# Kernel tuning notes

Measured on AMD Instinct MI355X. Metric: run time of the kernel, lower is better.

## Reference

```python
import jax, jax.numpy as jnp
import numpy as np

# irreps structure: in = 32x0e + 16x1o, hidden = 64x0e + 32x1o, out = 32x0e + 16x1o
N = 50000
S_IN, V_IN = 32, 16
S_H, V_H = 64, 32
S_OUT, V_OUT = 32, 16
INV_SQRT3 = float(1.0 / np.sqrt(3.0))  # wigner-3j for (0,1,1)/(1,0,1)/(1,1,0)
# e3nn path weights: sqrt(ir_out.dim / sum_over_paths_to_same_output(fan_in)), fan_in = mul1*mul2
PW1_S = float((1.0 / (S_IN * S_IN + V_IN * V_IN)) ** 0.5)        # sqrt(1/1280)
PW1_V = float((3.0 / (S_IN * V_IN + V_IN * S_IN)) ** 0.5)        # sqrt(3/1024)
PW2_S = float((1.0 / (S_H * S_H + V_H * V_H)) ** 0.5)            # sqrt(1/5120)
PW2_V = float((3.0 / (S_H * V_H + V_H * S_H)) ** 0.5)            # sqrt(3/4096)


def norm_act(xs, xv, bias=None, normalize=False):
    # e3nn.nn.NormActivation with sigmoid: per-irrep-channel norm, gate by sigmoid(norm [+ bias])
    ns = jnp.abs(xs)                                 # [N, S] scalar channel norms
    nv = jnp.sqrt(jnp.sum(xv * xv, axis=-1))         # [N, V] vector channel norms
    norms = jnp.concatenate([ns, nv], axis=1)        # [N, S+V]
    a = norms if bias is None else norms + bias
    f = jax.nn.sigmoid(a)
    mult = f / norms if normalize else f
    s = xs.shape[1]
    return xs * mult[:, :s], xv * mult[:, s:, None]


def fctp(xs, xv, Wsss, Wvvs, Wsvv, Wvsv, pw_s, pw_v):
    # FullyConnectedTensorProduct(x, x) restricted to 0e/1o irreps (all surviving CG paths)
    zs = pw_s * (jnp.einsum('nu,nv,uvw->nw', xs, xs, Wsss)
                 + INV_SQRT3 * jnp.einsum('nui,nvi,uvw->nw', xv, xv, Wvvs))
    zv = (pw_v * INV_SQRT3) * (jnp.einsum('nu,nvk,uvw->nwk', xs, xv, Wsvv)
                               + jnp.einsum('nuk,nv,uvw->nwk', xv, xs, Wvsv))
    return zs, zv


def setup_inputs() -> dict:
    key = jax.random.key(0)
    ks = jax.random.split(key, 11)
    return {
        'x': jax.random.normal(ks[0], (N, S_IN + 3 * V_IN), dtype=jnp.float32),
        'Wsss1': jax.random.normal(ks[1], (S_IN, S_IN, S_H), dtype=jnp.float32),
        'Wvvs1': jax.random.normal(ks[2], (V_IN, V_IN, S_H), dtype=jnp.float32),
        'Wsvv1': jax.random.normal(ks[3], (S_IN, V_IN, V_H), dtype=jnp.float32),
        'Wvsv1': jax.random.normal(ks[4], (V_IN, S_IN, V_H), dtype=jnp.float32),
        'Wsss2': jax.random.normal(ks[5], (S_H, S_H, S_OUT), dtype=jnp.float32),
        'Wvvs2': jax.random.normal(ks[6], (V_H, V_H, S_OUT), dtype=jnp.float32),
        'Wsvv2': jax.random.normal(ks[7], (S_H, V_H, V_OUT), dtype=jnp.float32),
        'Wvsv2': jax.random.normal(ks[8], (V_H, S_H, V_OUT), dtype=jnp.float32),
        'b1': 0.1 * jax.random.normal(ks[9], (S_IN + V_IN,), dtype=jnp.float32),
        'b3': 0.1 * jax.random.normal(ks[10], (S_OUT + V_OUT,), dtype=jnp.float32),
    }


def reference(x, Wsss1, Wvvs1, Wsvv1, Wvsv1, Wsss2, Wvvs2, Wsvv2, Wvsv2, b1, b3):
    xs = x[:, :S_IN]
    xv = x[:, S_IN:].reshape(-1, V_IN, 3)
    xs, xv = norm_act(xs, xv, bias=b1, normalize=False)            # non_linear_act1
    hs, hv = fctp(xs, xv, Wsss1, Wvvs1, Wsvv1, Wvsv1, PW1_S, PW1_V)  # si1
    hs, hv = norm_act(hs, hv, bias=None, normalize=True)           # normalize_and_non_linear_act2
    os_, ov = fctp(hs, hv, Wsss2, Wvvs2, Wsvv2, Wvsv2, PW2_S, PW2_V)  # si2
    os_, ov = norm_act(os_, ov, bias=b3, normalize=False)          # non_linear_act3
    return jnp.concatenate([os_, ov.reshape(-1, V_OUT * 3)], axis=1)
```

## Files before the change

kernel.cpp:

```cpp
#include <hip/hip_runtime.h>

#define NROWS 50000

typedef float f32x4 __attribute__((ext_vector_type(4)));
typedef float f32x16 __attribute__((ext_vector_type(16)));
typedef short s16x8 __attribute__((ext_vector_type(8)));
typedef _Float16 f16x8 __attribute__((ext_vector_type(8)));

#define MFMA16B(a,b,c) __builtin_amdgcn_mfma_f32_16x16x32_bf16(a, b, c, 0, 0, 0)
#define MFMA32B(a,b,c) __builtin_amdgcn_mfma_f32_32x32x16_bf16(a, b, c, 0, 0, 0)
#define MFMA32H(a,b,c) __builtin_amdgcn_mfma_f32_32x32x16_f16(a, b, c, 0, 0, 0)

#define Q1ABH 0
#define Q1ABL 81920
#define Q1CH  163840
#define Q1CL  212992
#define P2A   262144
#define P2C   425984
#define PREPN 393216


#define LO_SCALE   2048.0f
#define LO_UNSCALE 4.8828125e-4f

__device__ __forceinline__ float sigm(float a){ return 1.0f/(1.0f+__expf(-a)); }
__device__ __forceinline__ short bfb(float f){
  __bf16 b = (__bf16)f;
  return *reinterpret_cast<short*>(&b);
}
__device__ __forceinline__ float b2f(short s){
  unsigned u = ((unsigned)(unsigned short)s) << 16;
  float f;
  __builtin_memcpy(&f, &u, 4);
  return f;
}
__device__ __forceinline__ f32x16 zero16(){
  f32x16 v;
  #pragma unroll
  for (int i = 0; i < 16; ++i) v[i] = 0.f;
  return v;
}

__global__ __launch_bounds__(256) void prep_weights(
    const float* __restrict__ Wsss1, const float* __restrict__ Wvvs1,
    const float* __restrict__ Wsvv1, const float* __restrict__ Wvsv1,
    const float* __restrict__ Wsss2, const float* __restrict__ Wvvs2,
    const float* __restrict__ Wsvv2, const float* __restrict__ Wvsv2,
    short* __restrict__ pb)
{
  const float PW1S = 0.027950849718747374f;
  const float PW2S = 0.013975424859373687f;
  const float IS3  = 0.57735026918962576f;
  int i = blockIdx.x * 256 + threadIdx.x;
  if (i >= PREPN) return;
  if (i < 131072) {
    float w;
    int hiOff, loOff;
    if (i < 81920) {
      int e = i; int j = e & 7, l = (e >> 3) & 63, st = e >> 9;
      int t = st & 1, s = st >> 1;
      int k = 16*s + 8*(l >> 5) + j, n = 32*t + (l & 31);
      if (k < 1024) { int u = k >> 5, v = k & 31; w = PW1S * Wsss1[(u*32 + v)*64 + n]; }
      else { int kk = k - 1024; int u = kk >> 4, v = kk & 15; w = PW1S * IS3 * Wvvs1[(u*16 + v)*64 + n]; }
      hiOff = Q1ABH + e; loOff = Q1ABL + e;
    } else {
      int e = i - 81920; int e2 = e & 16383;
      int j = e2 & 7, l = (e2 >> 3) & 63, s = e2 >> 9;
      int k = 16*s + 8*(l >> 5) + j, n = l & 31;
      int u = k >> 4, v = k & 15;
      w = 0.03125f * (Wsvv1[(u*16 + v)*32 + n] + Wvsv1[(v*32 + u)*32 + n]);
      hiOff = Q1CH + e; loOff = Q1CL + e;
    }
    _Float16 h = (_Float16)w;
    float r = w - (float)h;
    _Float16 lo = (_Float16)(r * LO_SCALE);
    pb[hiOff] = *reinterpret_cast<short*>(&h);
    pb[loOff] = *reinterpret_cast<short*>(&lo);
  } else {
    int e = i - 131072;
    float val; int off;
    if (e < 163840) {
      int j = e & 7, l = (e >> 3) & 63, s = e >> 9;
      int k = 16*s + 8*(l >> 5) + j, n = l & 31;
      if (k < 4096) { int u = k >> 6, v = k & 63; val = PW2S * Wsss2[(u*64 + v)*32 + n]; }
      else { int kk = k - 4096; int u = kk >> 5, v = kk & 31; val = PW2S * IS3 * Wvvs2[(u*32 + v)*32 + n]; }
      off = P2A + e;
    } else {
      int e3 = e - 163840; int e4 = e3 & 32767;
      int j = e4 & 7, l = (e4 >> 3) & 63, s = e4 >> 9;
      int k = 32*s + 8*(l >> 4) + j, n = l & 15;
      int u = k >> 5, v = k & 31;
      val = 0.015625f * (Wsvv2[(u*32 + v)*16 + n] + Wvsv2[(v*64 + u)*16 + n]);
      off = P2C + e3;
    }
    pb[off] = bfb(val);
  }
}

__global__ __launch_bounds__(128, 4) void double_layer(
    const float* __restrict__ x,
    const float* __restrict__ b1,
    const float* __restrict__ b3,
    const short* __restrict__ pb,
    float* __restrict__ out)
{
  __shared__ __align__(16) float smem[5120];
  char* S = (char*)smem;

  const int lane = threadIdx.x & 63;
  const int wid  = __builtin_amdgcn_readfirstlane(threadIdx.x >> 6);
  const int h    = lane >> 5;
  const int r31  = lane & 31;
  const int row  = r31;
  const int grow0 = blockIdx.x * 32;
  const int xb = row * 320;
  const int hb = 10240 + row * 320;
  const int sz = ((row >> 1) & 3) << 4;
  const bool valid = (grow0 + row) < NROWS;
  const float* xrow = x + (size_t)(grow0 + row) * 80;

  if (wid == 0) {
    #pragma unroll
    for (int i = 0; i < 4; ++i) {
      float4 qv = valid ? ((const float4*)xrow)[4*h + i] : float4{0.f,0.f,0.f,0.f};
      int c0 = 16*h + 4*i;
      f32x4 o;
      o[0] = qv.x * sigm(fabsf(qv.x) + b1[c0+0]);
      o[1] = qv.y * sigm(fabsf(qv.y) + b1[c0+1]);
      o[2] = qv.z * sigm(fabsf(qv.z) + b1[c0+2]);
      o[3] = qv.w * sigm(fabsf(qv.w) + b1[c0+3]);
      *(f32x4*)(S + xb + ((64*h + 16*i) ^ sz)) = o;
    }
  } else {
    float t[24];
    #pragma unroll
    for (int i = 0; i < 6; ++i) {
      float4 qv = valid ? ((const float4*)xrow)[8 + 6*h + i] : float4{0.f,0.f,0.f,0.f};
      t[4*i] = qv.x; t[4*i+1] = qv.y; t[4*i+2] = qv.z; t[4*i+3] = qv.w;
    }
    #pragma unroll
    for (int vv = 0; vv < 8; ++vv) {
      float a0 = t[3*vv], a1 = t[3*vv+1], a2 = t[3*vv+2];
      float f = sigm(sqrtf(a0*a0 + a1*a1 + a2*a2) + b1[32 + 8*h + vv]);
      t[3*vv] = a0*f; t[3*vv+1] = a1*f; t[3*vv+2] = a2*f;
    }
    #pragma unroll
    for (int i = 0; i < 6; ++i) {
      f32x4 o; o[0] = t[4*i]; o[1] = t[4*i+1]; o[2] = t[4*i+2]; o[3] = t[4*i+3];
      *(f32x4*)(S + xb + ((128 + 96*h + 16*i) ^ sz)) = o;
    }
  }
  __syncthreads();

  if (wid == 0) {
    f32x16 aH0 = zero16(), aM0 = zero16(), aH1 = zero16(), aM1 = zero16();
    const f16x8* BH = (const f16x8*)(pb + Q1ABH);
    const f16x8* BL = (const f16x8*)(pb + Q1ABL);
    float xsv[16];
    {
      #pragma unroll
      for (int si = 0; si < 2; ++si) {
        f32x4 p0 = *(const f32x4*)(S + xb + ((64*si + 32*h) ^ sz));
        f32x4 p1 = *(const f32x4*)(S + xb + ((64*si + 32*h + 16) ^ sz));
        #pragma unroll
        for (int j = 0; j < 4; ++j) { xsv[8*si+j] = p0[j]; xsv[8*si+4+j] = p1[j]; }
      }
    }
    #pragma unroll 2
    for (int so = 0; so < 32; ++so) {
      float xu = *(const float*)(S + xb + ((4*so) ^ sz));
      #pragma unroll
      for (int si = 0; si < 2; ++si) {
        int s = 2*so + si;
        f16x8 ah, al;
        #pragma unroll
        for (int j = 0; j < 8; ++j) {
          float f = xu * xsv[8*si + j];
          _Float16 hh = (_Float16)f;
          ah[j] = hh;
          al[j] = (_Float16)((f - (float)hh) * LO_SCALE);
        }
        const f16x8* Bh = BH + (2*s)*64 + lane;
        const f16x8* Bl = BL + (2*s)*64 + lane;
        f16x8 b0 = Bh[0], b1_ = Bh[64];
        aH0 = MFMA32H(ah, b0,  aH0); aM0 = MFMA32H(al, b0,  aM0); aM0 = MFMA32H(ah, Bl[0],  aM0);
        aH1 = MFMA32H(ah, b1_, aH1); aM1 = MFMA32H(al, b1_, aM1); aM1 = MFMA32H(ah, Bl[64], aM1);
      }
    }
    {
      float pv0[8], pv1[8], pv2[8];
      f32x4 P[6];
      #pragma unroll
      for (int i = 0; i < 6; ++i) P[i] = *(const f32x4*)(S + xb + ((128 + 96*h + 16*i) ^ sz));
      #pragma unroll
      for (int j = 0; j < 8; ++j) {
        pv0[j] = P[(3*j  )>>2][(3*j  )&3];
        pv1[j] = P[(3*j+1)>>2][(3*j+1)&3];
        pv2[j] = P[(3*j+2)>>2][(3*j+2)&3];
      }
      #pragma unroll 2
      for (int s2 = 0; s2 < 16; ++s2) {
        int s = 64 + s2;
        float u0 = *(const float*)(S + xb + ((4*(32 + 3*s2    )) ^ sz));
        float u1 = *(const float*)(S + xb + ((4*(32 + 3*s2 + 1)) ^ sz));
        float u2 = *(const float*)(S + xb + ((4*(32 + 3*s2 + 2)) ^ sz));
        f16x8 ah, al;
        #pragma unroll
        for (int j = 0; j < 8; ++j) {
          float f = u0*pv0[j] + u1*pv1[j] + u2*pv2[j];
          _Float16 hh = (_Float16)f;
          ah[j] = hh;
          al[j] = (_Float16)((f - (float)hh) * LO_SCALE);
        }
        const f16x8* Bh = BH + (2*s)*64 + lane;
        const f16x8* Bl = BL + (2*s)*64 + lane;
        f16x8 b0 = Bh[0], b1_ = Bh[64];
        aH0 = MFMA32H(ah, b0,  aH0); aM0 = MFMA32H(al, b0,  aM0); aM0 = MFMA32H(ah, Bl[0],  aM0);
        aH1 = MFMA32H(ah, b1_, aH1); aM1 = MFMA32H(al, b1_, aM1); aM1 = MFMA32H(ah, Bl[64], aM1);
      }
    }
    #pragma unroll
    for (int reg = 0; reg < 16; ++reg) {
      int rowD = (reg & 3) + 8*(reg >> 2) + 4*h;
      int hbD = 10240 + rowD*320;
      int szD = ((rowD >> 1) & 3) << 4;
      float z0 = aH0[reg] + LO_UNSCALE*aM0[reg];
      float z1 = aH1[reg] + LO_UNSCALE*aM1[reg];
      *(short*)(S + hbD + ((2*r31)        ^ szD)) = bfb(copysignf(sigm(fabsf(z0)), z0));
      *(short*)(S + hbD + ((2*(32 + r31)) ^ szD)) = bfb(copysignf(sigm(fabsf(z1)), z1));
    }
  } else {
    float pv0[8], pv1[8], pv2[8];
    {
      f32x4 P[6];
      #pragma unroll
      for (int i = 0; i < 6; ++i) P[i] = *(const f32x4*)(S + xb + ((128 + 96*h + 16*i) ^ sz));
      #pragma unroll
      for (int j = 0; j < 8; ++j) {
        pv0[j] = P[(3*j  )>>2][(3*j  )&3];
        pv1[j] = P[(3*j+1)>>2][(3*j+1)&3];
        pv2[j] = P[(3*j+2)>>2][(3*j+2)&3];
      }
    }
    const f16x8* CH = (const f16x8*)(pb + Q1CH);
    const f16x8* CL = (const f16x8*)(pb + Q1CL);
    f32x16 z0v, z1v, z2v;
    {
      f32x16 cH0 = zero16(), cM0 = zero16(), cH1 = zero16(), cM1 = zero16();
      #pragma unroll 2
      for (int s = 0; s < 32; ++s) {
        float xu = *(const float*)(S + xb + ((4*s) ^ sz));
        f16x8 a0h, a0l, a1h, a1l;
        #pragma unroll
        for (int j = 0; j < 8; ++j) {
          float f0 = xu*pv0[j]; _Float16 h0 = (_Float16)f0; a0h[j] = h0; a0l[j] = (_Float16)((f0 - (float)h0)*LO_SCALE);
          float f1 = xu*pv1[j]; _Float16 h1 = (_Float16)f1; a1h[j] = h1; a1l[j] = (_Float16)((f1 - (float)h1)*LO_SCALE);
        }
        const f16x8* B0h = CH + s*64 + lane;
        const f16x8* B0l = CL + s*64 + lane;
        f16x8 t0 = B0h[0];
        cH0 = MFMA32H(a0h, t0, cH0); cM0 = MFMA32H(a0l, t0, cM0); cM0 = MFMA32H(a0h, B0l[0], cM0);
        f16x8 t1 = B0h[2048];
        cH1 = MFMA32H(a1h, t1, cH1); cM1 = MFMA32H(a1l, t1, cM1); cM1 = MFMA32H(a1h, B0l[2048], cM1);
      }
      #pragma unroll
      for (int i = 0; i < 16; ++i) { z0v[i] = cH0[i] + LO_UNSCALE*cM0[i]; z1v[i] = cH1[i] + LO_UNSCALE*cM1[i]; }
    }
    {
      f32x16 cH2 = zero16(), cM2 = zero16();
      #pragma unroll 2
      for (int s = 0; s < 32; ++s) {
        float xu = *(const float*)(S + xb + ((4*s) ^ sz));
        f16x8 a2h, a2l;
        #pragma unroll
        for (int j = 0; j < 8; ++j) {
          float f2 = xu*pv2[j]; _Float16 h2 = (_Float16)f2; a2h[j] = h2; a2l[j] = (_Float16)((f2 - (float)h2)*LO_SCALE);
        }
        const f16x8* B2h = CH + 4096 + s*64 + lane;
        const f16x8* B2l = CL + 4096 + s*64 + lane;
        f16x8 t2 = B2h[0];
        cH2 = MFMA32H(a2h, t2, cH2); cM2 = MFMA32H(a2l, t2, cM2); cM2 = MFMA32H(a2h, B2l[0], cM2);
      }
      #pragma unroll
      for (int i = 0; i < 16; ++i) z2v[i] = cH2[i] + LO_UNSCALE*cM2[i];
    }
    #pragma unroll
    for (int reg = 0; reg < 16; ++reg) {
      int rowD = (reg & 3) + 8*(reg >> 2) + 4*h;
      int hbD = 10240 + rowD*320;
      int szD = ((rowD >> 1) & 3) << 4;
      float a0 = z0v[reg], a1 = z1v[reg], a2 = z2v[reg];
      float n = sqrtf(a0*a0 + a1*a1 + a2*a2);
      float mm = sigm(n) / n;
      int ch = 64 + 3*r31;
      *(short*)(S + hbD + ((2*(ch    )) ^ szD)) = bfb(a0*mm);
      *(short*)(S + hbD + ((2*(ch + 1)) ^ szD)) = bfb(a1*mm);
      *(short*)(S + hbD + ((2*(ch + 2)) ^ szD)) = bfb(a2*mm);
    }
  }
  __syncthreads();

  if (wid == 0) {
    f32x16 acc = zero16();
    const s16x8* BA = (const s16x8*)(pb + P2A);
    {
      float hsv[32];
      #pragma unroll
      for (int p = 0; p < 4; ++p) {
        s16x8 w = *(const s16x8*)(S + hb + ((32*p + 16*h) ^ sz));
        #pragma unroll
        for (int j = 0; j < 8; ++j) hsv[8*p + j] = b2f(w[j]);
      }
      #pragma unroll 2
      for (int uu = 0; uu < 64; ++uu) {
        float hu = b2f(*(const short*)(S + hb + ((2*uu) ^ sz)));
        #pragma unroll
        for (int p = 0; p < 4; ++p) {
          s16x8 a;
          #pragma unroll
          for (int j = 0; j < 8; ++j) a[j] = bfb(hu * hsv[8*p + j]);
          acc = MFMA32B(a, BA[(4*uu + p)*64 + lane], acc);
        }
      }
    }
    {
      float hvv[48];
      #pragma unroll
      for (int p = 0; p < 2; ++p) {
        #pragma unroll
        for (int i = 0; i < 3; ++i) {
          s16x8 w = *(const s16x8*)(S + hb + ((128 + 96*p + 48*h + 16*i) ^ sz));
          #pragma unroll
          for (int j = 0; j < 8; ++j) hvv[24*p + 8*i + j] = b2f(w[j]);
        }
      }
      #pragma unroll 2
      for (int uu = 0; uu < 32; ++uu) {
        float u0 = b2f(*(const short*)(S + hb + ((2*(64 + 3*uu    )) ^ sz)));
        float u1 = b2f(*(const short*)(S + hb + ((2*(64 + 3*uu + 1)) ^ sz)));
        float u2 = b2f(*(const short*)(S + hb + ((2*(64 + 3*uu + 2)) ^ sz)));
        #pragma unroll
        for (int p = 0; p < 2; ++p) {
          s16x8 a;
          #pragma unroll
          for (int j = 0; j < 8; ++j) {
            float e0 = hvv[24*p + 3*j    ];
            float e1 = hvv[24*p + 3*j + 1];
            float e2 = hvv[24*p + 3*j + 2];
            a[j] = bfb(u0*e0 + u1*e1 + u2*e2);
          }
          acc = MFMA32B(a, BA[(256 + 2*uu + p)*64 + lane], acc);
        }
      }
    }
    float bs = b3[r31];
    #pragma unroll
    for (int reg = 0; reg < 16; ++reg) {
      int rowD = (reg & 3) + 8*(reg >> 2) + 4*h;
      int grow = grow0 + rowD;
      if (grow < NROWS) {
        float z = acc[reg];
        out[(size_t)grow*80 + r31] = z * sigm(fabsf(z) + bs);
      }
    }
  } else {
    const int q = lane >> 4, r15 = lane & 15;
    const int rA = r15, rB = 16 + r15;
    const int hbA = 10240 + rA*320, szA = ((rA >> 1) & 3) << 4;
    const int hbB = 10240 + rB*320, szB = ((rB >> 1) & 3) << 4;
    float vvA[24], vvB[24];
    #pragma unroll
    for (int i = 0; i < 3; ++i) {
      s16x8 wa = *(const s16x8*)(S + hbA + ((128 + 48*q + 16*i) ^ szA));
      s16x8 wb = *(const s16x8*)(S + hbB + ((128 + 48*q + 16*i) ^ szB));
      #pragma unroll
      for (int j = 0; j < 8; ++j) { vvA[8*i+j] = b2f(wa[j]); vvB[8*i+j] = b2f(wb[j]); }
    }
    f32x4 ac00 = {0.f,0.f,0.f,0.f}, ac01 = {0.f,0.f,0.f,0.f};
    f32x4 ac10 = {0.f,0.f,0.f,0.f}, ac11 = {0.f,0.f,0.f,0.f};
    f32x4 ac20 = {0.f,0.f,0.f,0.f}, ac21 = {0.f,0.f,0.f,0.f};
    const s16x8* BC = (const s16x8*)(pb + P2C);
    #pragma unroll 2
    for (int s = 0; s < 64; ++s) {
      float huA = b2f(*(const short*)(S + hbA + ((2*s) ^ szA)));
      float huB = b2f(*(const short*)(S + hbB + ((2*s) ^ szB)));
      s16x8 aA0, aA1, aA2, aB0, aB1, aB2;
      #pragma unroll
      for (int j = 0; j < 8; ++j) {
        aA0[j] = bfb(huA*vvA[3*j  ]); aA1[j] = bfb(huA*vvA[3*j+1]); aA2[j] = bfb(huA*vvA[3*j+2]);
        aB0[j] = bfb(huB*vvB[3*j  ]); aB1[j] = bfb(huB*vvB[3*j+1]); aB2[j] = bfb(huB*vvB[3*j+2]);
      }
      s16x8 B0 = BC[s*64 + lane];
      s16x8 B1 = BC[4096 + s*64 + lane];
      s16x8 B2 = BC[8192 + s*64 + lane];
      ac00 = MFMA16B(aA0, B0, ac00); ac01 = MFMA16B(aB0, B0, ac01);
      ac10 = MFMA16B(aA1, B1, ac10); ac11 = MFMA16B(aB1, B1, ac11);
      ac20 = MFMA16B(aA2, B2, ac20); ac21 = MFMA16B(aB2, B2, ac21);
    }
    float bv = b3[32 + r15];
    #pragma unroll
    for (int r = 0; r < 4; ++r) {
      int gA = grow0 + 4*q + r;
      if (gA < NROWS) {
        float z0 = ac00[r], z1 = ac10[r], z2 = ac20[r];
        float gg = sigm(sqrtf(z0*z0 + z1*z1 + z2*z2) + bv);
        out[(size_t)gA*80 + 32 + 3*r15    ] = z0*gg;
        out[(size_t)gA*80 + 32 + 3*r15 + 1] = z1*gg;
        out[(size_t)gA*80 + 32 + 3*r15 + 2] = z2*gg;
      }
      int gB = grow0 + 16 + 4*q + r;
      if (gB < NROWS) {
        float z0 = ac01[r], z1 = ac11[r], z2 = ac21[r];
        float gg = sigm(sqrtf(z0*z0 + z1*z1 + z2*z2) + bv);
        out[(size_t)gB*80 + 32 + 3*r15    ] = z0*gg;
        out[(size_t)gB*80 + 32 + 3*r15 + 1] = z1*gg;
        out[(size_t)gB*80 + 32 + 3*r15 + 2] = z2*gg;
      }
    }
  }
}

extern "C" void kernel_launch(void* const* d_in, const int* in_sizes, int n_in,
                              void* d_out, int out_size, void* d_ws, size_t ws_size,
                              hipStream_t stream) {
  const float* x     = (const float*)d_in[0];
  const float* Wsss1 = (const float*)d_in[1];
  const float* Wvvs1 = (const float*)d_in[2];
  const float* Wsvv1 = (const float*)d_in[3];
  const float* Wvsv1 = (const float*)d_in[4];
  const float* Wsss2 = (const float*)d_in[5];
  const float* Wvvs2 = (const float*)d_in[6];
  const float* Wsvv2 = (const float*)d_in[7];
  const float* Wvsv2 = (const float*)d_in[8];
  const float* b1    = (const float*)d_in[9];
  const float* b3    = (const float*)d_in[10];
  float* out = (float*)d_out;
  short* pb  = (short*)d_ws;

  hipLaunchKernelGGL(prep_weights, dim3((PREPN + 255)/256), dim3(256), 0, stream,
                     Wsss1, Wvvs1, Wsvv1, Wvsv1, Wsss2, Wvvs2, Wsvv2, Wvsv2, pb);
  hipLaunchKernelGGL(double_layer, dim3((NROWS + 31)/32), dim3(128), 0, stream,
                     x, b1, b3, pb, out);
}
```

Measured before the change: 122.1 us.

## Exploit symmetry of quadratic form in layer-2 scalar path to halve MFMAs

Because the scalar output of the second tensor product is a symmetric quadratic form in h (h_u h_v W_uvw), the prep kernel now folds W[u,v]+W[v,u] into upper-triangular 8x8 blocks. The wave-0 scalar path then iterates only over blocks with a<=b, for both the scalar-scalar and vector-vector parts. This roughly halves the MFMA count and the weight bytes loaded for that path. In exchange it adds a triangular block index decode in the prep kernel and a non-unrolled inner loop with a variable trip count in the main kernel.

```diff
diff --git a/kernel.cpp b/kernel.cpp
--- a/kernel.cpp
+++ b/kernel.cpp
@@ -16,8 +16,9 @@
 #define Q1CH  163840
 #define Q1CL  212992
 #define P2A   262144
+#define P2AV  (262144 + 73728)
 #define P2C   425984
-#define PREPN 393216
+#define PREPN 323584
 
 
 #define LO_SCALE   2048.0f
@@ -79,14 +80,31 @@
   } else {
     int e = i - 131072;
     float val; int off;
-    if (e < 163840) {
+    if (e < 73728) {
       int j = e & 7, l = (e >> 3) & 63, s = e >> 9;
       int k = 16*s + 8*(l >> 5) + j, n = l & 31;
-      if (k < 4096) { int u = k >> 6, v = k & 63; val = PW2S * Wsss2[(u*64 + v)*32 + n]; }
-      else { int kk = k - 4096; int u = kk >> 5, v = kk & 31; val = PW2S * IS3 * Wvvs2[(u*32 + v)*32 + n]; }
+      int B = k >> 6, kb = k & 63;
+      int bb = 0;
+      while ((bb + 1) * (bb + 2) / 2 <= B) ++bb;
+      int a = B - bb * (bb + 1) / 2;
+      int u = 8*a + (kb >> 3), v = 8*bb + (kb & 7);
+      float w1 = Wsss2[(u*64 + v)*32 + n];
+      val = PW2S * (a == bb ? w1 : w1 + Wsss2[(v*64 + u)*32 + n]);
       off = P2A + e;
+    } else if (e < 94208) {
+      int e2 = e - 73728;
+      int j = e2 & 7, l = (e2 >> 3) & 63, s = e2 >> 9;
+      int k = 16*s + 8*(l >> 5) + j, n = l & 31;
+      int B = k >> 6, kb = k & 63;
+      int bb = 0;
+      while ((bb + 1) * (bb + 2) / 2 <= B) ++bb;
+      int a = B - bb * (bb + 1) / 2;
+      int u = 8*a + (kb >> 3), v = 8*bb + (kb & 7);
+      float w1 = Wvvs2[(u*32 + v)*32 + n];
+      val = PW2S * IS3 * (a == bb ? w1 : w1 + Wvvs2[(v*32 + u)*32 + n]);
+      off = P2AV + e2;
     } else {
-      int e3 = e - 163840; int e4 = e3 & 32767;
+      int e3 = e - 94208; int e4 = e3 & 32767;
       int j = e4 & 7, l = (e4 >> 3) & 63, s = e4 >> 9;
       int k = 32*s + 8*(l >> 4) + j, n = l & 15;
       int u = k >> 5, v = k & 31;
@@ -302,54 +320,56 @@
 
   if (wid == 0) {
     f32x16 acc = zero16();
-    const s16x8* BA = (const s16x8*)(pb + P2A);
-    {
-      float hsv[32];
-      #pragma unroll
-      for (int p = 0; p < 4; ++p) {
-        s16x8 w = *(const s16x8*)(S + hb + ((32*p + 16*h) ^ sz));
-        #pragma unroll
-        for (int j = 0; j < 8; ++j) hsv[8*p + j] = b2f(w[j]);
-      }
+    {
+      const s16x8* BA = (const s16x8*)(pb + P2A);
+      int step = 0;
       #pragma unroll 2
-      for (int uu = 0; uu < 64; ++uu) {
-        float hu = b2f(*(const short*)(S + hb + ((2*uu) ^ sz)));
-        #pragma unroll
-        for (int p = 0; p < 4; ++p) {
-          s16x8 a;
+      for (int b = 0; b < 8; ++b) {
+        float hsb[8];
+        {
+          s16x8 w = *(const s16x8*)(S + hb + ((16*b) ^ sz));
           #pragma unroll
-          for (int j = 0; j < 8; ++j) a[j] = bfb(hu * hsv[8*p + j]);
-          acc = MFMA32B(a, BA[(4*uu + p)*64 + lane], acc);
-        }
-      }
-    }
-    {
-      float hvv[48];
-      #pragma unroll
-      for (int p = 0; p < 2; ++p) {
+          for (int j = 0; j < 8; ++j) hsb[j] = b2f(w[j]);
+        }
+        for (int a = 0; a <= b; ++a) {
+          #pragma unroll
+          for (int s4 = 0; s4 < 4; ++s4) {
+            float hu = b2f(*(const short*)(S + hb + ((2*(8*a + 2*s4 + h)) ^ sz)));
+            s16x8 av;
+            #pragma unroll
+            for (int j = 0; j < 8; ++j) av[j] = bfb(hu * hsb[j]);
+            acc = MFMA32B(av, BA[step*64 + lane], acc);
+            ++step;
+          }
+        }
+      }
+    }
+    {
+      const s16x8* BV = (const s16x8*)(pb + P2AV);
+      int step = 0;
+      #pragma unroll
+      for (int b = 0; b < 4; ++b) {
+        float hvb[24];
         #pragma unroll
         for (int i = 0; i < 3; ++i) {
-          s16x8 w = *(const s16x8*)(S + hb + ((128 + 96*p + 48*h + 16*i) ^ sz));
+          s16x8 w = *(const s16x8*)(S + hb + ((2*(64 + 24*b + 8*i)) ^ sz));
           #pragma unroll
-          for (int j = 0; j < 8; ++j) hvv[24*p + 8*i + j] = b2f(w[j]);
-        }
-      }
-      #pragma unroll 2
-      for (int uu = 0; uu < 32; ++uu) {
-        float u0 = b2f(*(const short*)(S + hb + ((2*(64 + 3*uu    )) ^ sz)));
-        float u1 = b2f(*(const short*)(S + hb + ((2*(64 + 3*uu + 1)) ^ sz)));
-        float u2 = b2f(*(const short*)(S + hb + ((2*(64 + 3*uu + 2)) ^ sz)));
-        #pragma unroll
-        for (int p = 0; p < 2; ++p) {
-          s16x8 a;
+          for (int j = 0; j < 8; ++j) hvb[8*i + j] = b2f(w[j]);
+        }
+        for (int a = 0; a <= b; ++a) {
           #pragma unroll
-          for (int j = 0; j < 8; ++j) {
-            float e0 = hvv[24*p + 3*j    ];
-            float e1 = hvv[24*p + 3*j + 1];
-            float e2 = hvv[24*p + 3*j + 2];
-            a[j] = bfb(u0*e0 + u1*e1 + u2*e2);
+          for (int s4 = 0; s4 < 4; ++s4) {
+            int u = 8*a + 2*s4 + h;
+            float u0 = b2f(*(const short*)(S + hb + ((2*(64 + 3*u    )) ^ sz)));
+            float u1 = b2f(*(const short*)(S + hb + ((2*(64 + 3*u + 1)) ^ sz)));
+            float u2 = b2f(*(const short*)(S + hb + ((2*(64 + 3*u + 2)) ^ sz)));
+            s16x8 av;
+            #pragma unroll
+            for (int j = 0; j < 8; ++j)
+              av[j] = bfb(u0*hvb[3*j] + u1*hvb[3*j+1] + u2*hvb[3*j+2]);
+            acc = MFMA32B(av, BV[step*64 + lane], acc);
+            ++step;
           }
-          acc = MFMA32B(a, BA[(256 + 2*uu + p)*64 + lane], acc);
         }
       }
     }
```

After: 116.2 us. -4.9%, faster.
